# Kernel optimization log

Hardware: AMD Instinct MI355X
Metric: run time of the kernel (lower is better)

Reference implementation:

```python
import jax, jax.numpy as jnp
import numpy as np

N = 50000          # number of nodes
NNZ = 800000       # edges per relation (avg degree 16)
R = 3              # edge_features / number of relations
D_IN = 128
D_OUT = 128
EPS = 1e-6


def setup_inputs() -> dict:
    key = jax.random.key(0)
    ks = jax.random.split(key, 8)
    return {
        "input": jax.random.normal(ks[0], (N, D_IN), dtype=jnp.float32),
        "adj_rows": jax.random.randint(ks[1], (R, NNZ), 0, N, dtype=jnp.int64) if jax.config.jax_enable_x64 else jax.random.randint(ks[1], (R, NNZ), 0, N).astype(jnp.int32),
        "adj_cols": jax.random.randint(ks[2], (R, NNZ), 0, N, dtype=jnp.int64) if jax.config.jax_enable_x64 else jax.random.randint(ks[2], (R, NNZ), 0, N).astype(jnp.int32),
        "adj_vals": jax.random.uniform(ks[3], (R, NNZ), dtype=jnp.float32),
        "weight": jax.random.normal(ks[4], (D_IN * R, D_OUT), dtype=jnp.float32) * (1.0 / np.sqrt(D_OUT)),
        "share_weight": jax.random.normal(ks[5], (D_IN, D_OUT), dtype=jnp.float32) * (1.0 / np.sqrt(D_OUT)),
        "bias": jax.random.normal(ks[6], (D_OUT,), dtype=jnp.float32) * (1.0 / np.sqrt(D_OUT)),
        "ln_gamma": jnp.ones((D_IN,), dtype=jnp.float32),
        "ln_beta": jnp.zeros((D_IN,), dtype=jnp.float32),
    }


def _spmm(rows, cols, vals, x, n_nodes):
    # (sparse A) @ x via gather + segment-sum: out[r] = sum_{e: rows[e]=r} vals[e]*x[cols[e]]
    msgs = vals[:, None] * x[cols]            # [nnz, d]
    return jax.ops.segment_sum(msgs, rows, num_segments=n_nodes)


def _layernorm(x, gamma, beta):
    mu = jnp.mean(x, axis=-1, keepdims=True)
    var = jnp.var(x, axis=-1, keepdims=True)
    return (x - mu) * jax.lax.rsqrt(var + EPS) * gamma + beta


def reference(input, adj_rows, adj_cols, adj_vals, weight, share_weight, bias, ln_gamma, ln_beta):
    n = input.shape[0]
    # loop over the small fixed relation set to keep peak memory low
    support_list = [
        _spmm(adj_rows[r], adj_cols[r], adj_vals[r], input, n) for r in range(adj_rows.shape[0])
    ]
    support = jnp.concatenate(support_list, axis=1)   # [N, R*d_in]
    support_sum = support_list[0]
    for s in support_list[1:]:
        support_sum = support_sum + s
    support_norm = _layernorm(support_sum, ln_gamma, ln_beta)
    out = (support @ weight + support_norm @ share_weight) * 0.5
    return out + bias
```

## Files before the change

kernel.cpp:

```cpp
#include <hip/hip_runtime.h>
#include <hip/hip_fp16.h>

constexpr int NN  = 50000;
constexpr int NNZ = 800000;
constexpr int RR  = 3;
constexpr int D   = 128;
constexpr int RN  = RR * NN;
constexpr int NE  = RR * NNZ;
constexpr int KK  = 512;
constexpr int MPAD = 50048;
constexpr int PART = 256;
constexpr int PSZ  = (RN + PART - 1) / PART;
constexpr int CAP  = 10240;
constexpr int EPB  = 2048;
constexpr int CAPB = 24;
constexpr float EPS = 1e-6f;

constexpr int NB_SPLIT = (NE + EPB - 1) / EPB;
constexpr int NB_XH    = (NN * 64 + 255) / 256;
constexpr int NB_WT    = 256;

using bf16x8 = __attribute__((ext_vector_type(8))) __bf16;
using f32x4  = __attribute__((ext_vector_type(4))) float;

__device__ __forceinline__ unsigned pack_bf2(float a, float b) {
  unsigned ua = __float_as_uint(a); ua = (ua + (0x7FFFu + ((ua >> 16) & 1))) >> 16;
  unsigned ub = __float_as_uint(b); ub = (ub + (0x7FFFu + ((ub >> 16) & 1))) >> 16;
  return ua | (ub << 16);
}
__device__ __forceinline__ unsigned bf16_lo(float a) {
  unsigned ua = __float_as_uint(a);
  return (ua + (0x7FFFu + ((ua >> 16) & 1))) >> 16;
}

__device__ __forceinline__ void gload16(const void* g, void* l) {
  __builtin_amdgcn_global_load_lds(
      (const __attribute__((address_space(1))) unsigned int*)g,
      (__attribute__((address_space(3))) unsigned int*)l, 16, 0, 0);
}

__device__ __forceinline__ float val16(unsigned u) {
  return __half2float(__ushort_as_half((unsigned short)(u & 0xFFFFu)));
}

#define ACC2(accA, accB, word, vv) {                                   \
    __half2 _h = __builtin_bit_cast(__half2, (word));                  \
    accA = __builtin_fmaf(__half2float(_h.x), (vv), accA);             \
    accB = __builtin_fmaf(__half2float(_h.y), (vv), accB); }

__global__ __launch_bounds__(256) void prep(
    const int*   __restrict__ rows,
    const int*   __restrict__ cols,
    const float* __restrict__ vals,
    const float* __restrict__ x,
    const float* __restrict__ w,
    const float* __restrict__ shw,
    int*   __restrict__ pcur,
    uint2* __restrict__ pedges,
    unsigned* __restrict__ xh,
    unsigned short* __restrict__ WT) {
  __shared__ int lcur[PART], lbase[PART];
  __shared__ uint2 lbuf[PART][CAPB];
  int blk = blockIdx.x;
  int t = threadIdx.x;

  if (blk >= NB_SPLIT) {
    int b2 = blk - NB_SPLIT;
    if (b2 < NB_XH) {
      int i = b2 * 256 + t;
      float2 v = ((const float2*)x)[i];
      xh[i] = __builtin_bit_cast(unsigned, __floats2half2_rn(v.x, v.y));
    } else {
      int idx = (b2 - NB_XH) * 256 + t;
      int k   = idx >> 7;
      int col = idx & 127;
      float v = (k < 384) ? w[k * 128 + col] : shw[(k - 384) * 128 + col];
      WT[col * 512 + k] = (unsigned short)bf16_lo(v);
    }
    return;
  }

  lcur[t] = 0;
  __syncthreads();
  int e0 = blk * EPB;
  constexpr int EPT = EPB / 256;
  int ovf_pe[EPT], ovf_rank[EPT];
  uint2 ovf_val[EPT];
  #pragma unroll
  for (int j = 0; j < EPT; j++) {
    ovf_pe[j] = -1;
    int e = e0 + j * 256 + t;
    if (e < NE) {
      int r = (e >= 2 * NNZ) ? 2 : (e >= NNZ ? 1 : 0);
      int b = r * NN + rows[e];
      int p = b / PSZ;
      unsigned pay = ((unsigned)cols[e] << 16) |
                     (unsigned)__half_as_ushort(__float2half_rn(vals[e]));
      int rank = atomicAdd(&lcur[p], 1);
      if (rank < CAPB) {
        lbuf[p][rank] = make_uint2((unsigned)b, pay);
      } else {
        ovf_pe[j] = p; ovf_rank[j] = rank;
        ovf_val[j] = make_uint2((unsigned)b, pay);
      }
    }
  }
  __syncthreads();
  lbase[t] = atomicAdd(&pcur[t], lcur[t]);
  __syncthreads();
  int wid = t >> 6, l = t & 63;
  for (int q = 0; q < 64; q++) {
    int p = wid * 64 + q;
    int n = min(lcur[p], CAPB);
    uint2* dst = pedges + (size_t)p * CAP + lbase[p];
    for (int i = l; i < n; i += 64) dst[i] = lbuf[p][i];
  }
  #pragma unroll
  for (int j = 0; j < EPT; j++)
    if (ovf_pe[j] >= 0)
      pedges[(size_t)ovf_pe[j] * CAP + lbase[ovf_pe[j]] + ovf_rank[j]] = ovf_val[j];
}

__global__ __launch_bounds__(256) void sort_part(
    const uint2* __restrict__ pedges,
    const int*   __restrict__ pcur,
    int* __restrict__ off,
    unsigned* __restrict__ epack) {
  __shared__ int sc[PSZ];
  __shared__ int sdata[256];
  int p = blockIdx.x;
  int t = threadIdx.x;
  int bb = p * PSZ;
  int nbuck = min(PSZ, RN - bb);
  int n = pcur[p];
  const uint2* src = pedges + (size_t)p * CAP;

  sdata[t] = (t < p) ? pcur[t] : 0;
  __syncthreads();
  #pragma unroll
  for (int step = 128; step >= 1; step >>= 1) {
    if (t < step) sdata[t] += sdata[t + step];
    __syncthreads();
  }
  int gbase = sdata[0];
  __syncthreads();
  if (p == 0 && t == 0) off[RN] = NE;

  for (int i = t; i < nbuck; i += 256) sc[i] = 0;
  __syncthreads();
  for (int i = t; i < n; i += 256)
    atomicAdd(&sc[src[i].x - bb], 1);
  __syncthreads();

  constexpr int PER = (PSZ + 255) / 256;
  int lo = t * PER, hi = min(lo + PER, nbuck);
  int s = 0;
  for (int i = lo; i < hi; i++) s += sc[i];
  sdata[t] = s;
  __syncthreads();
  #pragma unroll
  for (int step = 1; step < 256; step <<= 1) {
    int v = (t >= step) ? sdata[t - step] : 0;
    __syncthreads();
    sdata[t] += v;
    __syncthreads();
  }
  int run = gbase + sdata[t] - s;
  for (int i = lo; i < hi; i++) {
    int c = sc[i];
    sc[i] = run;
    off[bb + i] = run;
    run += c;
  }
  __syncthreads();

  for (int i = t; i < n; i += 256) {
    uint2 ed = src[i];
    int pos = atomicAdd(&sc[ed.x - bb], 1);
    epack[pos] = ed.y;
  }
}

__global__ __launch_bounds__(256) void gather_ln(
    const unsigned* __restrict__ xh,
    const unsigned* __restrict__ epack,
    const int*      __restrict__ off,
    const float* __restrict__ gamma,
    const float* __restrict__ beta,
    unsigned* __restrict__ Au) {
  int node = blockIdx.x * 4 + (threadIdx.x >> 6);
  if (node >= NN) return;
  int lane = threadIdx.x & 63;
  int g  = lane >> 4;
  int q  = lane & 15;
  const unsigned* xq = xh + q * 4;

  float l0=0,l1=0,l2=0,l3=0,l4=0,l5=0,l6=0,l7=0;

  #pragma unroll
  for (int r = 0; r < RR; r++) {
    int b = r * NN + node;
    int s = off[b], e2 = off[b + 1];
    float a0=0,a1=0,a2=0,a3=0,a4=0,a5=0,a6=0,a7=0;

    for (int i0 = s; i0 < e2; i0 += 64) {
      int navail = min(64, e2 - i0);
      unsigned ep = (lane < navail) ? epack[i0 + lane] : 0u;
      int c0 = 0;
      for (; c0 + 16 <= navail; c0 += 16) {
        unsigned ua = __shfl(ep, c0 + g);
        unsigned ub = __shfl(ep, c0 + 4 + g);
        unsigned uc = __shfl(ep, c0 + 8 + g);
        unsigned ud = __shfl(ep, c0 + 12 + g);
        uint4 ga = *(const uint4*)(xq + (size_t)(ua >> 16) * 64);
        uint4 gb = *(const uint4*)(xq + (size_t)(ub >> 16) * 64);
        uint4 gc = *(const uint4*)(xq + (size_t)(uc >> 16) * 64);
        uint4 gd = *(const uint4*)(xq + (size_t)(ud >> 16) * 64);
        float va = val16(ua), vb = val16(ub), vc = val16(uc), vd = val16(ud);
        ACC2(a0,a1,ga.x,va) ACC2(a2,a3,ga.y,va) ACC2(a4,a5,ga.z,va) ACC2(a6,a7,ga.w,va)
        ACC2(a0,a1,gb.x,vb) ACC2(a2,a3,gb.y,vb) ACC2(a4,a5,gb.z,vb) ACC2(a6,a7,gb.w,vb)
        ACC2(a0,a1,gc.x,vc) ACC2(a2,a3,gc.y,vc) ACC2(a4,a5,gc.z,vc) ACC2(a6,a7,gc.w,vc)
        ACC2(a0,a1,gd.x,vd) ACC2(a2,a3,gd.y,vd) ACC2(a4,a5,gd.z,vd) ACC2(a6,a7,gd.w,vd)
      }
      for (; c0 + 4 <= navail; c0 += 4) {
        unsigned u = __shfl(ep, c0 + g);
        uint4 gg = *(const uint4*)(xq + (size_t)(u >> 16) * 64);
        float v = val16(u);
        ACC2(a0,a1,gg.x,v) ACC2(a2,a3,gg.y,v) ACC2(a4,a5,gg.z,v) ACC2(a6,a7,gg.w,v)
      }
      if (c0 < navail) {
        int eidx = c0 + g;
        unsigned u = __shfl(ep, min(eidx, navail - 1));
        float v = (eidx < navail) ? val16(u) : 0.0f;
        uint4 gg = *(const uint4*)(xq + (size_t)(u >> 16) * 64);
        ACC2(a0,a1,gg.x,v) ACC2(a2,a3,gg.y,v) ACC2(a4,a5,gg.z,v) ACC2(a6,a7,gg.w,v)
      }
    }
    #define REDG(x) x += __shfl_xor(x, 16); x += __shfl_xor(x, 32);
    REDG(a0) REDG(a1) REDG(a2) REDG(a3) REDG(a4) REDG(a5) REDG(a6) REDG(a7)
    #undef REDG
    if (g == 0) {
      uint4 w;
      w.x = pack_bf2(a0, a1); w.y = pack_bf2(a2, a3);
      w.z = pack_bf2(a4, a5); w.w = pack_bf2(a6, a7);
      *(uint4*)(Au + (size_t)node * 256 + r * 64 + q * 4) = w;
    }
    l0 += a0; l1 += a1; l2 += a2; l3 += a3;
    l4 += a4; l5 += a5; l6 += a6; l7 += a7;
  }

  float sum = l0+l1+l2+l3+l4+l5+l6+l7;
  float sq  = l0*l0+l1*l1+l2*l2+l3*l3+l4*l4+l5*l5+l6*l6+l7*l7;
  #pragma unroll
  for (int m = 1; m <= 8; m <<= 1) {
    sum += __shfl_xor(sum, m);
    sq  += __shfl_xor(sq,  m);
  }
  float mean = sum * (1.0f / D);
  float var  = sq * (1.0f / D) - mean * mean;
  float rstd = rsqrtf(var + EPS);
  float4 gm0 = *(const float4*)&gamma[8 * q];
  float4 gm1 = *(const float4*)&gamma[8 * q + 4];
  float4 bt0 = *(const float4*)&beta[8 * q];
  float4 bt1 = *(const float4*)&beta[8 * q + 4];
  float o0 = (l0 - mean) * rstd * gm0.x + bt0.x;
  float o1 = (l1 - mean) * rstd * gm0.y + bt0.y;
  float o2 = (l2 - mean) * rstd * gm0.z + bt0.z;
  float o3 = (l3 - mean) * rstd * gm0.w + bt0.w;
  float o4 = (l4 - mean) * rstd * gm1.x + bt1.x;
  float o5 = (l5 - mean) * rstd * gm1.y + bt1.y;
  float o6 = (l6 - mean) * rstd * gm1.z + bt1.z;
  float o7 = (l7 - mean) * rstd * gm1.w + bt1.w;
  if (g == 0) {
    uint4 w;
    w.x = pack_bf2(o0, o1); w.y = pack_bf2(o2, o3);
    w.z = pack_bf2(o4, o5); w.w = pack_bf2(o6, o7);
    *(uint4*)(Au + (size_t)node * 256 + 192 + q * 4) = w;
  }
}

__global__ __launch_bounds__(512) void gemm_mfma(
    const char* __restrict__ Ab,
    const char* __restrict__ Bb,
    const float* __restrict__ bias,
    float* __restrict__ out) {
  __shared__ __align__(16) char smem[32768];
  char* As = smem;
  char* Bs = smem + 16384;

  int tid  = threadIdx.x;
  int wid  = tid >> 6;
  int lane = tid & 63;
  int wr   = wid >> 1;
  int wc   = wid & 1;
  int row0 = blockIdx.x * 128;

  f32x4 zero = {0.f, 0.f, 0.f, 0.f};
  f32x4 acc[2][4];
  #pragma unroll
  for (int i = 0; i < 2; i++)
    #pragma unroll
    for (int j = 0; j < 4; j++) acc[i][j] = zero;

  for (int kc = 0; kc < 8; kc++) {
    #pragma unroll
    for (int i = 0; i < 2; i++) {
      int c = i * 512 + tid;
      int r = c >> 3, s = c & 7;
      int ss = s ^ (r & 7);
      const void* src = Ab + (size_t)(row0 + r) * 1024 + kc * 128 + ss * 16;
      void* dst = As + i * 8192 + wid * 1024;
      gload16(src, dst);
    }
    #pragma unroll
    for (int i = 0; i < 2; i++) {
      int c = i * 512 + tid;
      int r = c >> 3, s = c & 7;
      int ss = s ^ (r & 7);
      const void* src = Bb + (size_t)r * 1024 + kc * 128 + ss * 16;
      void* dst = Bs + i * 8192 + wid * 1024;
      gload16(src, dst);
    }
    __syncthreads();

    #pragma unroll
    for (int ks = 0; ks < 2; ks++) {
      bf16x8 afrag[2], bfrag[4];
      int sg = ks * 4 + (lane >> 4);
      #pragma unroll
      for (int rb = 0; rb < 2; rb++) {
        int r = wr * 32 + rb * 16 + (lane & 15);
        afrag[rb] = *(const bf16x8*)(As + r * 128 + (sg ^ (r & 7)) * 16);
      }
      #pragma unroll
      for (int cb = 0; cb < 4; cb++) {
        int col = wc * 64 + cb * 16 + (lane & 15);
        bfrag[cb] = *(const bf16x8*)(Bs + col * 128 + (sg ^ (col & 7)) * 16);
      }
      #pragma unroll
      for (int rb = 0; rb < 2; rb++)
        #pragma unroll
        for (int cb = 0; cb < 4; cb++)
          acc[rb][cb] = __builtin_amdgcn_mfma_f32_16x16x32_bf16(
              afrag[rb], bfrag[cb], acc[rb][cb], 0, 0, 0);
    }
    __syncthreads();
  }

  #pragma unroll
  for (int rb = 0; rb < 2; rb++) {
    #pragma unroll
    for (int cb = 0; cb < 4; cb++) {
      int col = wc * 64 + cb * 16 + (lane & 15);
      float bv = bias[col];
      #pragma unroll
      for (int r = 0; r < 4; r++) {
        int grow = row0 + wr * 32 + rb * 16 + (lane >> 4) * 4 + r;
        if (grow < NN) out[(size_t)grow * 128 + col] = 0.5f * acc[rb][cb][r] + bv;
      }
    }
  }
}

extern "C" void kernel_launch(void* const* d_in, const int* in_sizes, int n_in,
                              void* d_out, int out_size, void* d_ws, size_t ws_size,
                              hipStream_t stream) {
  const float* input  = (const float*)d_in[0];
  const int*   arows  = (const int*)  d_in[1];
  const int*   acols  = (const int*)  d_in[2];
  const float* avals  = (const float*)d_in[3];
  const float* weight = (const float*)d_in[4];
  const float* shw    = (const float*)d_in[5];
  const float* bias   = (const float*)d_in[6];
  const float* gamma  = (const float*)d_in[7];
  const float* beta   = (const float*)d_in[8];
  float* out = (float*)d_out;

  char* ws = (char*)d_ws;
  char*  Abf   = ws;                         ws += (size_t)MPAD * KK * 2;
  unsigned short* WT = (unsigned short*)ws;  ws += (size_t)128 * KK * 2;
  unsigned* xh  = (unsigned*)ws;             ws += (size_t)NN * 64 * 4;
  uint2* pedges = (uint2*)ws;                ws += (size_t)PART * CAP * sizeof(uint2);
  unsigned* epack = (unsigned*)ws;           ws += (size_t)NE * 4;
  int*   off   = (int*)ws;                   ws += ((size_t)RN + 4) * sizeof(int);
  int*   pcur  = (int*)ws;                   ws += (size_t)PART * sizeof(int);

  hipMemsetAsync(pcur, 0, (size_t)PART * sizeof(int), stream);
  prep      <<<NB_SPLIT + NB_XH + NB_WT, 256, 0, stream>>>(
                arows, acols, avals, input, weight, shw, pcur, pedges, xh, WT);
  sort_part <<<PART, 256, 0, stream>>>(pedges, pcur, off, epack);
  gather_ln <<<(NN + 3) / 4, 256, 0, stream>>>(xh, epack, off, gamma, beta,
                                               (unsigned*)Abf);
  gemm_mfma <<<MPAD / 128, 512, 0, stream>>>(Abf, (const char*)WT, bias, out);
}
```

Before: 178.7 us.

## Split feature gather into two column-half passes and widen sort blocks

```diff
diff --git a/kernel.cpp b/kernel.cpp
--- a/kernel.cpp
+++ b/kernel.cpp
@@ -57,7 +57,8 @@
     const float* __restrict__ shw,
     int*   __restrict__ pcur,
     uint2* __restrict__ pedges,
-    unsigned* __restrict__ xh,
+    unsigned* __restrict__ xlo,
+    unsigned* __restrict__ xhi,
     unsigned short* __restrict__ WT) {
   __shared__ int lcur[PART], lbase[PART];
   __shared__ uint2 lbuf[PART][CAPB];
@@ -69,7 +70,10 @@
     if (b2 < NB_XH) {
       int i = b2 * 256 + t;
       float2 v = ((const float2*)x)[i];
-      xh[i] = __builtin_bit_cast(unsigned, __floats2half2_rn(v.x, v.y));
+      unsigned pv = __builtin_bit_cast(unsigned, __floats2half2_rn(v.x, v.y));
+      int node = i >> 6, ww = i & 63;
+      if (ww < 32) xlo[node * 32 + ww] = pv;
+      else         xhi[node * 32 + (ww - 32)] = pv;
     } else {
       int idx = (b2 - NB_XH) * 256 + t;
       int k   = idx >> 7;
@@ -121,13 +125,13 @@
       pedges[(size_t)ovf_pe[j] * CAP + lbase[ovf_pe[j]] + ovf_rank[j]] = ovf_val[j];
 }
 
-__global__ __launch_bounds__(256) void sort_part(
+__global__ __launch_bounds__(512) void sort_part(
     const uint2* __restrict__ pedges,
     const int*   __restrict__ pcur,
     int* __restrict__ off,
     unsigned* __restrict__ epack) {
   __shared__ int sc[PSZ];
-  __shared__ int sdata[256];
+  __shared__ int sdata[512];
   int p = blockIdx.x;
   int t = threadIdx.x;
   int bb = p * PSZ;
@@ -135,10 +139,10 @@
   int n = pcur[p];
   const uint2* src = pedges + (size_t)p * CAP;
 
-  sdata[t] = (t < p) ? pcur[t] : 0;
-  __syncthreads();
-  #pragma unroll
-  for (int step = 128; step >= 1; step >>= 1) {
+  sdata[t] = (t < p && t < PART) ? pcur[t] : 0;
+  __syncthreads();
+  #pragma unroll
+  for (int step = 256; step >= 1; step >>= 1) {
     if (t < step) sdata[t] += sdata[t + step];
     __syncthreads();
   }
@@ -146,20 +150,20 @@
   __syncthreads();
   if (p == 0 && t == 0) off[RN] = NE;
 
-  for (int i = t; i < nbuck; i += 256) sc[i] = 0;
-  __syncthreads();
-  for (int i = t; i < n; i += 256)
+  for (int i = t; i < nbuck; i += 512) sc[i] = 0;
+  __syncthreads();
+  for (int i = t; i < n; i += 512)
     atomicAdd(&sc[src[i].x - bb], 1);
   __syncthreads();
 
-  constexpr int PER = (PSZ + 255) / 256;
+  constexpr int PER = (PSZ + 511) / 512;
   int lo = t * PER, hi = min(lo + PER, nbuck);
   int s = 0;
   for (int i = lo; i < hi; i++) s += sc[i];
   sdata[t] = s;
   __syncthreads();
   #pragma unroll
-  for (int step = 1; step < 256; step <<= 1) {
+  for (int step = 1; step < 512; step <<= 1) {
     int v = (t >= step) ? sdata[t - step] : 0;
     __syncthreads();
     sdata[t] += v;
@@ -174,34 +178,36 @@
   }
   __syncthreads();
 
-  for (int i = t; i < n; i += 256) {
+  for (int i = t; i < n; i += 512) {
     uint2 ed = src[i];
     int pos = atomicAdd(&sc[ed.x - bb], 1);
     epack[pos] = ed.y;
   }
 }
 
-__global__ __launch_bounds__(256) void gather_ln(
-    const unsigned* __restrict__ xh,
+template <int HALF>
+__global__ __launch_bounds__(256) void gather_half(
+    const unsigned* __restrict__ xt,
     const unsigned* __restrict__ epack,
     const int*      __restrict__ off,
     const float* __restrict__ gamma,
     const float* __restrict__ beta,
+    float* __restrict__ slabsum_lo,
     unsigned* __restrict__ Au) {
   int node = blockIdx.x * 4 + (threadIdx.x >> 6);
   if (node >= NN) return;
   int lane = threadIdx.x & 63;
   int g  = lane >> 4;
   int q  = lane & 15;
-  const unsigned* xq = xh + q * 4;
-
-  float l0=0,l1=0,l2=0,l3=0,l4=0,l5=0,l6=0,l7=0;
+  const unsigned* xq = xt + q * 2;
+
+  float l0=0,l1=0,l2=0,l3=0;
 
   #pragma unroll
   for (int r = 0; r < RR; r++) {
     int b = r * NN + node;
     int s = off[b], e2 = off[b + 1];
-    float a0=0,a1=0,a2=0,a3=0,a4=0,a5=0,a6=0,a7=0;
+    float a0=0,a1=0,a2=0,a3=0;
 
     for (int i0 = s; i0 < e2; i0 += 64) {
       int navail = min(64, e2 - i0);
@@ -212,45 +218,51 @@
         unsigned ub = __shfl(ep, c0 + 4 + g);
         unsigned uc = __shfl(ep, c0 + 8 + g);
         unsigned ud = __shfl(ep, c0 + 12 + g);
-        uint4 ga = *(const uint4*)(xq + (size_t)(ua >> 16) * 64);
-        uint4 gb = *(const uint4*)(xq + (size_t)(ub >> 16) * 64);
-        uint4 gc = *(const uint4*)(xq + (size_t)(uc >> 16) * 64);
-        uint4 gd = *(const uint4*)(xq + (size_t)(ud >> 16) * 64);
+        uint2 ga = *(const uint2*)(xq + (size_t)(ua >> 16) * 32);
+        uint2 gb = *(const uint2*)(xq + (size_t)(ub >> 16) * 32);
+        uint2 gc = *(const uint2*)(xq + (size_t)(uc >> 16) * 32);
+        uint2 gd = *(const uint2*)(xq + (size_t)(ud >> 16) * 32);
         float va = val16(ua), vb = val16(ub), vc = val16(uc), vd = val16(ud);
-        ACC2(a0,a1,ga.x,va) ACC2(a2,a3,ga.y,va) ACC2(a4,a5,ga.z,va) ACC2(a6,a7,ga.w,va)
-        ACC2(a0,a1,gb.x,vb) ACC2(a2,a3,gb.y,vb) ACC2(a4,a5,gb.z,vb) ACC2(a6,a7,gb.w,vb)
-        ACC2(a0,a1,gc.x,vc) ACC2(a2,a3,gc.y,vc) ACC2(a4,a5,gc.z,vc) ACC2(a6,a7,gc.w,vc)
-        ACC2(a0,a1,gd.x,vd) ACC2(a2,a3,gd.y,vd) ACC2(a4,a5,gd.z,vd) ACC2(a6,a7,gd.w,vd)
+        ACC2(a0,a1,ga.x,va) ACC2(a2,a3,ga.y,va)
+        ACC2(a0,a1,gb.x,vb) ACC2(a2,a3,gb.y,vb)
+        ACC2(a0,a1,gc.x,vc) ACC2(a2,a3,gc.y,vc)
+        ACC2(a0,a1,gd.x,vd) ACC2(a2,a3,gd.y,vd)
       }
       for (; c0 + 4 <= navail; c0 += 4) {
         unsigned u = __shfl(ep, c0 + g);
-        uint4 gg = *(const uint4*)(xq + (size_t)(u >> 16) * 64);
+        uint2 gg = *(const uint2*)(xq + (size_t)(u >> 16) * 32);
         float v = val16(u);
-        ACC2(a0,a1,gg.x,v) ACC2(a2,a3,gg.y,v) ACC2(a4,a5,gg.z,v) ACC2(a6,a7,gg.w,v)
+        ACC2(a0,a1,gg.x,v) ACC2(a2,a3,gg.y,v)
       }
       if (c0 < navail) {
         int eidx = c0 + g;
         unsigned u = __shfl(ep, min(eidx, navail - 1));
         float v = (eidx < navail) ? val16(u) : 0.0f;
-        uint4 gg = *(const uint4*)(xq + (size_t)(u >> 16) * 64);
-        ACC2(a0,a1,gg.x,v) ACC2(a2,a3,gg.y,v) ACC2(a4,a5,gg.z,v) ACC2(a6,a7,gg.w,v)
+        uint2 gg = *(const uint2*)(xq + (size_t)(u >> 16) * 32);
+        ACC2(a0,a1,gg.x,v) ACC2(a2,a3,gg.y,v)
       }
     }
     #define REDG(x) x += __shfl_xor(x, 16); x += __shfl_xor(x, 32);
-    REDG(a0) REDG(a1) REDG(a2) REDG(a3) REDG(a4) REDG(a5) REDG(a6) REDG(a7)
+    REDG(a0) REDG(a1) REDG(a2) REDG(a3)
     #undef REDG
     if (g == 0) {
-      uint4 w;
-      w.x = pack_bf2(a0, a1); w.y = pack_bf2(a2, a3);
-      w.z = pack_bf2(a4, a5); w.w = pack_bf2(a6, a7);
-      *(uint4*)(Au + (size_t)node * 256 + r * 64 + q * 4) = w;
+      uint2 wv = make_uint2(pack_bf2(a0, a1), pack_bf2(a2, a3));
+      *(uint2*)(Au + (size_t)node * 256 + r * 64 + HALF * 32 + q * 2) = wv;
     }
     l0 += a0; l1 += a1; l2 += a2; l3 += a3;
-    l4 += a4; l5 += a5; l6 += a6; l7 += a7;
-  }
-
-  float sum = l0+l1+l2+l3+l4+l5+l6+l7;
-  float sq  = l0*l0+l1*l1+l2*l2+l3*l3+l4*l4+l5*l5+l6*l6+l7*l7;
+  }
+
+  if (HALF == 0) {
+    if (g == 0)
+      *(float4*)(slabsum_lo + (size_t)node * 64 + q * 4) =
+          make_float4(l0, l1, l2, l3);
+    return;
+  }
+
+  float4 slo = *(const float4*)(slabsum_lo + (size_t)node * 64 + q * 4);
+  float sum = l0 + l1 + l2 + l3 + slo.x + slo.y + slo.z + slo.w;
+  float sq  = l0*l0 + l1*l1 + l2*l2 + l3*l3
+            + slo.x*slo.x + slo.y*slo.y + slo.z*slo.z + slo.w*slo.w;
   #pragma unroll
   for (int m = 1; m <= 8; m <<= 1) {
     sum += __shfl_xor(sum, m);
@@ -259,23 +271,23 @@
   float mean = sum * (1.0f / D);
   float var  = sq * (1.0f / D) - mean * mean;
   float rstd = rsqrtf(var + EPS);
-  float4 gm0 = *(const float4*)&gamma[8 * q];
-  float4 gm1 = *(const float4*)&gamma[8 * q + 4];
-  float4 bt0 = *(const float4*)&beta[8 * q];
-  float4 bt1 = *(const float4*)&beta[8 * q + 4];
-  float o0 = (l0 - mean) * rstd * gm0.x + bt0.x;
-  float o1 = (l1 - mean) * rstd * gm0.y + bt0.y;
-  float o2 = (l2 - mean) * rstd * gm0.z + bt0.z;
-  float o3 = (l3 - mean) * rstd * gm0.w + bt0.w;
-  float o4 = (l4 - mean) * rstd * gm1.x + bt1.x;
-  float o5 = (l5 - mean) * rstd * gm1.y + bt1.y;
-  float o6 = (l6 - mean) * rstd * gm1.z + bt1.z;
-  float o7 = (l7 - mean) * rstd * gm1.w + bt1.w;
+  float4 gl = *(const float4*)&gamma[q * 4];
+  float4 bl = *(const float4*)&beta[q * 4];
+  float4 gh = *(const float4*)&gamma[64 + q * 4];
+  float4 bh = *(const float4*)&beta[64 + q * 4];
+  float lo0 = (slo.x - mean) * rstd * gl.x + bl.x;
+  float lo1 = (slo.y - mean) * rstd * gl.y + bl.y;
+  float lo2 = (slo.z - mean) * rstd * gl.z + bl.z;
+  float lo3 = (slo.w - mean) * rstd * gl.w + bl.w;
+  float hi0 = (l0 - mean) * rstd * gh.x + bh.x;
+  float hi1 = (l1 - mean) * rstd * gh.y + bh.y;
+  float hi2 = (l2 - mean) * rstd * gh.z + bh.z;
+  float hi3 = (l3 - mean) * rstd * gh.w + bh.w;
   if (g == 0) {
-    uint4 w;
-    w.x = pack_bf2(o0, o1); w.y = pack_bf2(o2, o3);
-    w.z = pack_bf2(o4, o5); w.w = pack_bf2(o6, o7);
-    *(uint4*)(Au + (size_t)node * 256 + 192 + q * 4) = w;
+    *(uint2*)(Au + (size_t)node * 256 + 192 + q * 2) =
+        make_uint2(pack_bf2(lo0, lo1), pack_bf2(lo2, lo3));
+    *(uint2*)(Au + (size_t)node * 256 + 192 + 32 + q * 2) =
+        make_uint2(pack_bf2(hi0, hi1), pack_bf2(hi2, hi3));
   }
 }
 
@@ -379,17 +391,23 @@
   char* ws = (char*)d_ws;
   char*  Abf   = ws;                         ws += (size_t)MPAD * KK * 2;
   unsigned short* WT = (unsigned short*)ws;  ws += (size_t)128 * KK * 2;
-  unsigned* xh  = (unsigned*)ws;             ws += (size_t)NN * 64 * 4;
+  unsigned* xlo = (unsigned*)ws;             ws += (size_t)NN * 32 * 4;
+  unsigned* xhi = (unsigned*)ws;             ws += (size_t)NN * 32 * 4;
   uint2* pedges = (uint2*)ws;                ws += (size_t)PART * CAP * sizeof(uint2);
   unsigned* epack = (unsigned*)ws;           ws += (size_t)NE * 4;
   int*   off   = (int*)ws;                   ws += ((size_t)RN + 4) * sizeof(int);
   int*   pcur  = (int*)ws;                   ws += (size_t)PART * sizeof(int);
 
+  float* slabsum_lo = (float*)pedges;
+
   hipMemsetAsync(pcur, 0, (size_t)PART * sizeof(int), stream);
   prep      <<<NB_SPLIT + NB_XH + NB_WT, 256, 0, stream>>>(
-                arows, acols, avals, input, weight, shw, pcur, pedges, xh, WT);
-  sort_part <<<PART, 256, 0, stream>>>(pedges, pcur, off, epack);
-  gather_ln <<<(NN + 3) / 4, 256, 0, stream>>>(xh, epack, off, gamma, beta,
-                                               (unsigned*)Abf);
+                arows, acols, avals, input, weight, shw, pcur, pedges,
+                xlo, xhi, WT);
+  sort_part <<<PART, 512, 0, stream>>>(pedges, pcur, off, epack);
+  gather_half<0><<<(NN + 3) / 4, 256, 0, stream>>>(
+                xlo, epack, off, gamma, beta, slabsum_lo, (unsigned*)Abf);
+  gather_half<1><<<(NN + 3) / 4, 256, 0, stream>>>(
+                xhi, epack, off, gamma, beta, slabsum_lo, (unsigned*)Abf);
   gemm_mfma <<<MPAD / 128, 512, 0, stream>>>(Abf, (const char*)WT, bias, out);
 }
```

New measurement: 201.6 us. +12.8%, slower.
